# Kernel tuning notes

Hardware: AMD Instinct MI355X
Metric: run time of the kernel (lower is better)

## Reference

```python
import jax, jax.numpy as jnp
import numpy as np


def _splat_one(inp, fx, fy):
    """Bilinear forward-splat one sample.
    inp: [C1, H, W] values to scatter; fx, fy: [H, W] destination coords.
    Returns [C1, H, W] scatter-add accumulation.
    """
    C1, H, W = inp.shape
    inp_flat = inp.reshape(C1, H * W)  # [C1, HW]
    out = jnp.zeros((C1, H * W), dtype=inp.dtype)
    x0 = jnp.floor(fx).astype(jnp.int32)
    y0 = jnp.floor(fy).astype(jnp.int32)
    for dx in (0, 1):
        for dy in (0, 1):
            xi = x0 + dx
            yi = y0 + dy
            # bilinear weight to this corner
            w = (1.0 - jnp.abs(fx - xi.astype(fx.dtype))) * (1.0 - jnp.abs(fy - yi.astype(fy.dtype)))
            valid = (xi >= 0) & (xi < W) & (yi >= 0) & (yi < H)
            w = jnp.where(valid, w, 0.0).reshape(-1)  # [HW]
            idx = (jnp.clip(yi, 0, H - 1) * W + jnp.clip(xi, 0, W - 1)).reshape(-1)
            out = out.at[:, idx].add(inp_flat * w[None, :])
    return out.reshape(C1, H, W)


def softsplat_soft(img, flow, metric):
    """Softmax splatting (FunctionSoftsplat, mode='soft').
    img [B,C,H,W], flow [B,2,H,W] (ch0=x disp, ch1=y disp), metric [B,1,H,W].
    """
    B, C, H, W = img.shape
    weight = jnp.exp(metric)                      # [B,1,H,W]
    inp = jnp.concatenate([img * weight, weight], axis=1)  # [B,C+1,H,W]
    gx = jnp.arange(W, dtype=img.dtype)[None, None, :]
    gy = jnp.arange(H, dtype=img.dtype)[None, :, None]
    fx = flow[:, 0] + gx                          # [B,H,W]
    fy = flow[:, 1] + gy                          # [B,H,W]
    acc = jax.vmap(_splat_one)(inp, fx, fy)       # [B,C+1,H,W]
    norm = acc[:, C:C + 1]
    norm = jnp.where(norm == 0.0, 1.0, norm)      # avoid div-by-zero (matches original)
    return acc[:, :C] / norm


def setup_inputs() -> dict:
    key = jax.random.key(0)
    k1, k2, k3 = jax.random.split(key, 3)
    B, C, H, W = 8, 3, 1024, 1024
    img = jax.random.uniform(k1, (B, C, H, W), dtype=jnp.float32)
    flow = jax.random.normal(k2, (B, 2, H, W), dtype=jnp.float32) * 4.0
    metric = jax.random.normal(k3, (B, 1, H, W), dtype=jnp.float32)
    return {"img": img, "flow": flow, "metric": metric}


def reference(img, flow, metric):
    return softsplat_soft(img, flow, metric)
```

## Files before the change

kernel.cpp:

```cpp
#include <hip/hip_runtime.h>

constexpr int B_ = 8;
constexpr int H_ = 1024;
constexpr int W_ = 1024;
constexpr int HW_ = H_ * W_;

constexpr int TW = 64;
constexpr int TH = 64;
constexpr int R  = 24;
constexpr int WX = TW + 2 * R;
constexpr int WY = TH + 2 * R;
constexpr int NT = 512;
constexpr int LSTRIDE = TW + 1;

__global__ __launch_bounds__(256) void outlier_kernel(
    const float* __restrict__ img,
    const float* __restrict__ flow,
    const float* __restrict__ metric,
    int* __restrict__ counter,
    float4* __restrict__ rec_vals,
    int* __restrict__ rec_cells,
    int cap)
{
    const int t = blockIdx.x * 256 + threadIdx.x;
    if (t >= B_ * HW_) return;
    const int b = t >> 20;
    const int p = t & (HW_ - 1);
    const int y = p >> 10;
    const int x = p & (W_ - 1);

    const float fx = flow[(size_t)(b * 2 + 0) * HW_ + p] + (float)x;
    const float fy = flow[(size_t)(b * 2 + 1) * HW_ + p] + (float)y;
    const float x0f = floorf(fx);
    const float y0f = floorf(fy);
    const int x0 = (int)x0f;
    const int y0 = (int)y0f;

    const bool far = (abs(x0 - x) > R) || (abs(x0 + 1 - x) > R) ||
                     (abs(y0 - y) > R) || (abs(y0 + 1 - y) > R);
    if (!far) return;

    const float wgt = __expf(metric[(size_t)b * HW_ + p]);
    const float v0 = img[(size_t)(b * 3 + 0) * HW_ + p] * wgt;
    const float v1 = img[(size_t)(b * 3 + 1) * HW_ + p] * wgt;
    const float v2 = img[(size_t)(b * 3 + 2) * HW_ + p] * wgt;
    const float wx1 = fx - x0f, wx0 = 1.0f - wx1;
    const float wy1 = fy - y0f, wy0 = 1.0f - wy1;

#pragma unroll
    for (int dy = 0; dy < 2; ++dy) {
        const int yi = y0 + dy;
        if (yi < 0 || yi >= H_) continue;
#pragma unroll
        for (int dx = 0; dx < 2; ++dx) {
            const int xi = x0 + dx;
            if (xi < 0 || xi >= W_) continue;
            if (abs(xi - x) <= R && abs(yi - y) <= R) continue;
            const float w = (dx ? wx1 : wx0) * (dy ? wy1 : wy0);
            const int idx = atomicAdd(counter, 1);
            if (idx < cap) {
                rec_cells[idx] = (b << 20) | (yi << 10) | xi;
                rec_vals[idx]  = make_float4(v0 * w, v1 * w, v2 * w, wgt * w);
            }
        }
    }
}

__global__ __launch_bounds__(NT) void splat_tile_kernel(
    const float* __restrict__ img,
    const float* __restrict__ flow,
    const float* __restrict__ metric,
    float* __restrict__ out,
    const int* __restrict__ counter,
    const float4* __restrict__ rec_vals,
    const int* __restrict__ rec_cells,
    int cap)
{
    __shared__ float acc[4][TH][LSTRIDE];

    const int tid = threadIdx.x;
    const int tx0 = blockIdx.x * TW;
    const int ty0 = blockIdx.y * TH;
    const int b   = blockIdx.z;

    float* const a = &acc[0][0][0];
    for (int i = tid; i < 4 * TH * LSTRIDE; i += NT) a[i] = 0.0f;
    __syncthreads();

    const float* const flowx = flow + (size_t)(b * 2 + 0) * HW_;
    const float* const flowy = flow + (size_t)(b * 2 + 1) * HW_;
    const float* const metr  = metric + (size_t)b * HW_;
    const float* const img0  = img + (size_t)(b * 3 + 0) * HW_;
    const float* const img1  = img + (size_t)(b * 3 + 1) * HW_;
    const float* const img2  = img + (size_t)(b * 3 + 2) * HW_;

    for (int i = tid; i < WX * WY; i += NT) {
        const int wy = i / WX;
        const int wx = i - wy * WX;
        const int sx = tx0 - R + wx;
        const int sy = ty0 - R + wy;
        if (sx < 0 || sx >= W_ || sy < 0 || sy >= H_) continue;
        const int p = (sy << 10) + sx;

        const float fx = flowx[p] + (float)sx;
        const float fy = flowy[p] + (float)sy;
        const float x0f = floorf(fx);
        const float y0f = floorf(fy);
        const int x0 = (int)x0f;
        const int y0 = (int)y0f;

        if (x0 + 1 < tx0 || x0 > tx0 + TW - 1 ||
            y0 + 1 < ty0 || y0 > ty0 + TH - 1) continue;

        const float wgt = __expf(metr[p]);
        const float v0 = img0[p] * wgt;
        const float v1 = img1[p] * wgt;
        const float v2 = img2[p] * wgt;
        const float wx1 = fx - x0f, wx0f_ = 1.0f - wx1;
        const float wy1 = fy - y0f, wy0f_ = 1.0f - wy1;

#pragma unroll
        for (int dy = 0; dy < 2; ++dy) {
            const int yi = y0 + dy;
            const int ly = yi - ty0;
            if ((unsigned)ly >= TH) continue;
#pragma unroll
            for (int dx = 0; dx < 2; ++dx) {
                const int xi = x0 + dx;
                const int lx = xi - tx0;
                if ((unsigned)lx >= TW) continue;
                if (abs(xi - sx) > R || abs(yi - sy) > R) continue;
                const float w = (dx ? wx1 : wx0f_) * (dy ? wy1 : wy0f_);
                atomicAdd(&acc[0][ly][lx], v0 * w);
                atomicAdd(&acc[1][ly][lx], v1 * w);
                atomicAdd(&acc[2][ly][lx], v2 * w);
                atomicAdd(&acc[3][ly][lx], wgt * w);
            }
        }
    }
    __syncthreads();

    const int n = min(*counter, cap);
    for (int r = tid; r < n; r += NT) {
        const int cell = rec_cells[r];
        const int rb = cell >> 20;
        if (rb != b) continue;
        const int q  = cell & (HW_ - 1);
        const int yi = q >> 10;
        const int xi = q & (W_ - 1);
        const int ly = yi - ty0;
        const int lx = xi - tx0;
        if ((unsigned)ly >= TH || (unsigned)lx >= TW) continue;
        const float4 v = rec_vals[r];
        atomicAdd(&acc[0][ly][lx], v.x);
        atomicAdd(&acc[1][ly][lx], v.y);
        atomicAdd(&acc[2][ly][lx], v.z);
        atomicAdd(&acc[3][ly][lx], v.w);
    }
    __syncthreads();

    for (int i = tid; i < TH * TW; i += NT) {
        const int ly = i >> 6;
        const int lx = i & (TW - 1);
        const float wsum = acc[3][ly][lx];
        const float inv = (wsum == 0.0f) ? 1.0f : 1.0f / wsum;
        const int q = ((ty0 + ly) << 10) + (tx0 + lx);
        out[(size_t)(b * 3 + 0) * HW_ + q] = acc[0][ly][lx] * inv;
        out[(size_t)(b * 3 + 1) * HW_ + q] = acc[1][ly][lx] * inv;
        out[(size_t)(b * 3 + 2) * HW_ + q] = acc[2][ly][lx] * inv;
    }
}

extern "C" void kernel_launch(void* const* d_in, const int* in_sizes, int n_in,
                              void* d_out, int out_size, void* d_ws, size_t ws_size,
                              hipStream_t stream)
{
    const float* img    = (const float*)d_in[0];
    const float* flow   = (const float*)d_in[1];
    const float* metric = (const float*)d_in[2];
    float* out = (float*)d_out;

    int* counter = (int*)d_ws;
    long long avail = (long long)ws_size - 64;
    int cap = (int)min((long long)(1 << 22), avail > 0 ? avail / 20 : 0);
    float4* rec_vals = (float4*)((char*)d_ws + 64);
    int* rec_cells = (int*)((char*)d_ws + 64 + (size_t)cap * sizeof(float4));

    hipMemsetAsync(counter, 0, 64, stream);

    {
        const int n = B_ * HW_;
        outlier_kernel<<<(n + 255) / 256, 256, 0, stream>>>(
            img, flow, metric, counter, rec_vals, rec_cells, cap);
    }
    {
        dim3 grid(W_ / TW, H_ / TH, B_);
        splat_tile_kernel<<<grid, NT, 0, stream>>>(
            img, flow, metric, out, counter, rec_vals, rec_cells, cap);
    }
}
```

Before: 710.7 us.

## Precompute fp16-packed weighted values in prepass, shrink halo, vectorize loads and stores

The prepass now also computes exp(metric)-weighted image values and packs them as four fp16 numbers per pixel into a workspace buffer. The tile kernel then reads one 8-byte value and only gathers it for pixels that land in the tile, instead of reading metric plus three image channels. The halo radius drops from 24 to 16, which shrinks the window each tile scans but pushes more pixels into the global outlier list. That list's capacity is also cut to a fixed 65536, which risks silent overflow with flow std 4. Flow loads, prepass loads and output stores are vectorized to float4, and fp16 storage of the weighted values costs precision.

```diff
diff --git a/kernel.cpp b/kernel.cpp
--- a/kernel.cpp
+++ b/kernel.cpp
@@ -1,4 +1,5 @@
 #include <hip/hip_runtime.h>
+#include <hip/hip_fp16.h>
 
 constexpr int B_ = 8;
 constexpr int H_ = 1024;
@@ -7,74 +8,104 @@
 
 constexpr int TW = 64;
 constexpr int TH = 64;
-constexpr int R  = 24;
+constexpr int R  = 16;
 constexpr int WX = TW + 2 * R;
 constexpr int WY = TH + 2 * R;
+constexpr int GPR = WX / 4;
+constexpr int NGROUPS = GPR * WY;
 constexpr int NT = 512;
 constexpr int LSTRIDE = TW + 1;
 
-__global__ __launch_bounds__(256) void outlier_kernel(
+constexpr int CAP = 65536;
+
+constexpr size_t OFF_VALS  = 64;
+constexpr size_t OFF_CELLS = OFF_VALS + (size_t)CAP * 16;
+constexpr size_t OFF_VAL   = OFF_CELLS + (size_t)CAP * 4;
+
+__global__ __launch_bounds__(256) void prepass_kernel(
     const float* __restrict__ img,
     const float* __restrict__ flow,
     const float* __restrict__ metric,
+    uint2* __restrict__ val,
     int* __restrict__ counter,
     float4* __restrict__ rec_vals,
-    int* __restrict__ rec_cells,
-    int cap)
+    int* __restrict__ rec_cells)
 {
     const int t = blockIdx.x * 256 + threadIdx.x;
-    if (t >= B_ * HW_) return;
-    const int b = t >> 20;
-    const int p = t & (HW_ - 1);
-    const int y = p >> 10;
-    const int x = p & (W_ - 1);
-
-    const float fx = flow[(size_t)(b * 2 + 0) * HW_ + p] + (float)x;
-    const float fy = flow[(size_t)(b * 2 + 1) * HW_ + p] + (float)y;
-    const float x0f = floorf(fx);
-    const float y0f = floorf(fy);
-    const int x0 = (int)x0f;
-    const int y0 = (int)y0f;
-
-    const bool far = (abs(x0 - x) > R) || (abs(x0 + 1 - x) > R) ||
-                     (abs(y0 - y) > R) || (abs(y0 + 1 - y) > R);
-    if (!far) return;
-
-    const float wgt = __expf(metric[(size_t)b * HW_ + p]);
-    const float v0 = img[(size_t)(b * 3 + 0) * HW_ + p] * wgt;
-    const float v1 = img[(size_t)(b * 3 + 1) * HW_ + p] * wgt;
-    const float v2 = img[(size_t)(b * 3 + 2) * HW_ + p] * wgt;
-    const float wx1 = fx - x0f, wx0 = 1.0f - wx1;
-    const float wy1 = fy - y0f, wy0 = 1.0f - wy1;
-
-#pragma unroll
-    for (int dy = 0; dy < 2; ++dy) {
-        const int yi = y0 + dy;
-        if (yi < 0 || yi >= H_) continue;
-#pragma unroll
-        for (int dx = 0; dx < 2; ++dx) {
-            const int xi = x0 + dx;
-            if (xi < 0 || xi >= W_) continue;
-            if (abs(xi - x) <= R && abs(yi - y) <= R) continue;
-            const float w = (dx ? wx1 : wx0) * (dy ? wy1 : wy0);
-            const int idx = atomicAdd(counter, 1);
-            if (idx < cap) {
-                rec_cells[idx] = (b << 20) | (yi << 10) | xi;
-                rec_vals[idx]  = make_float4(v0 * w, v1 * w, v2 * w, wgt * w);
+    if (t >= B_ * HW_ / 4) return;
+    const int b  = t >> 18;
+    const int p4 = (t & (HW_ / 4 - 1)) << 2;
+    const int y  = p4 >> 10;
+    const int x0p = p4 & (W_ - 1);
+
+    const float4 m4  = *(const float4*)(metric + (size_t)b * HW_ + p4);
+    const float4 i0  = *(const float4*)(img + (size_t)(b * 3 + 0) * HW_ + p4);
+    const float4 i1  = *(const float4*)(img + (size_t)(b * 3 + 1) * HW_ + p4);
+    const float4 i2  = *(const float4*)(img + (size_t)(b * 3 + 2) * HW_ + p4);
+    const float4 fx4 = *(const float4*)(flow + (size_t)(b * 2 + 0) * HW_ + p4);
+    const float4 fy4 = *(const float4*)(flow + (size_t)(b * 2 + 1) * HW_ + p4);
+
+    uint2 packed[4];
+    const float mv[4] = {m4.x, m4.y, m4.z, m4.w};
+    const float a0[4] = {i0.x, i0.y, i0.z, i0.w};
+    const float a1[4] = {i1.x, i1.y, i1.z, i1.w};
+    const float a2[4] = {i2.x, i2.y, i2.z, i2.w};
+    const float fxa[4] = {fx4.x, fx4.y, fx4.z, fx4.w};
+    const float fya[4] = {fy4.x, fy4.y, fy4.z, fy4.w};
+
+#pragma unroll
+    for (int k = 0; k < 4; ++k) {
+        const float wgt = __expf(mv[k]);
+        const float v0 = a0[k] * wgt;
+        const float v1 = a1[k] * wgt;
+        const float v2 = a2[k] * wgt;
+        const __half2 h01 = __floats2half2_rn(v0, v1);
+        const __half2 h23 = __floats2half2_rn(v2, wgt);
+        packed[k].x = *(const unsigned int*)&h01;
+        packed[k].y = *(const unsigned int*)&h23;
+
+        const int x = x0p + k;
+        const float fx = fxa[k] + (float)x;
+        const float fy = fya[k] + (float)y;
+        const float x0f = floorf(fx);
+        const float y0f = floorf(fy);
+        const int x0 = (int)x0f;
+        const int y0 = (int)y0f;
+        const bool far = (abs(x0 - x) > R) || (abs(x0 + 1 - x) > R) ||
+                         (abs(y0 - y) > R) || (abs(y0 + 1 - y) > R);
+        if (far) {
+            const float wx1 = fx - x0f, wx0 = 1.0f - wx1;
+            const float wy1 = fy - y0f, wy0 = 1.0f - wy1;
+#pragma unroll
+            for (int dy = 0; dy < 2; ++dy) {
+                const int yi = y0 + dy;
+                if (yi < 0 || yi >= H_) continue;
+#pragma unroll
+                for (int dx = 0; dx < 2; ++dx) {
+                    const int xi = x0 + dx;
+                    if (xi < 0 || xi >= W_) continue;
+                    if (abs(xi - x) <= R && abs(yi - y) <= R) continue;
+                    const float w = (dx ? wx1 : wx0) * (dy ? wy1 : wy0);
+                    const int idx = atomicAdd(counter, 1);
+                    if (idx < CAP) {
+                        rec_cells[idx] = (b << 20) | (yi << 10) | xi;
+                        rec_vals[idx]  = make_float4(v0 * w, v1 * w, v2 * w, wgt * w);
+                    }
+                }
             }
         }
     }
+    *(reinterpret_cast<uint4*>(val + (size_t)b * HW_ + p4))     = *(uint4*)&packed[0];
+    *(reinterpret_cast<uint4*>(val + (size_t)b * HW_ + p4) + 1) = *(uint4*)&packed[2];
 }
 
 __global__ __launch_bounds__(NT) void splat_tile_kernel(
-    const float* __restrict__ img,
     const float* __restrict__ flow,
-    const float* __restrict__ metric,
+    const uint2* __restrict__ val,
     float* __restrict__ out,
     const int* __restrict__ counter,
     const float4* __restrict__ rec_vals,
-    const int* __restrict__ rec_cells,
-    int cap)
+    const int* __restrict__ rec_cells)
 {
     __shared__ float acc[4][TH][LSTRIDE];
 
@@ -89,35 +120,23 @@
 
     const float* const flowx = flow + (size_t)(b * 2 + 0) * HW_;
     const float* const flowy = flow + (size_t)(b * 2 + 1) * HW_;
-    const float* const metr  = metric + (size_t)b * HW_;
-    const float* const img0  = img + (size_t)(b * 3 + 0) * HW_;
-    const float* const img1  = img + (size_t)(b * 3 + 1) * HW_;
-    const float* const img2  = img + (size_t)(b * 3 + 2) * HW_;
-
-    for (int i = tid; i < WX * WY; i += NT) {
-        const int wy = i / WX;
-        const int wx = i - wy * WX;
-        const int sx = tx0 - R + wx;
-        const int sy = ty0 - R + wy;
-        if (sx < 0 || sx >= W_ || sy < 0 || sy >= H_) continue;
-        const int p = (sy << 10) + sx;
-
-        const float fx = flowx[p] + (float)sx;
-        const float fy = flowy[p] + (float)sy;
+    const uint2* const valb  = val + (size_t)b * HW_;
+
+    auto process = [&](float fx, float fy, int sx, int sy) {
         const float x0f = floorf(fx);
         const float y0f = floorf(fy);
         const int x0 = (int)x0f;
         const int y0 = (int)y0f;
-
         if (x0 + 1 < tx0 || x0 > tx0 + TW - 1 ||
-            y0 + 1 < ty0 || y0 > ty0 + TH - 1) continue;
-
-        const float wgt = __expf(metr[p]);
-        const float v0 = img0[p] * wgt;
-        const float v1 = img1[p] * wgt;
-        const float v2 = img2[p] * wgt;
-        const float wx1 = fx - x0f, wx0f_ = 1.0f - wx1;
-        const float wy1 = fy - y0f, wy0f_ = 1.0f - wy1;
+            y0 + 1 < ty0 || y0 > ty0 + TH - 1) return;
+
+        const uint2 u = valb[(sy << 10) + sx];
+        const float2 f01 = __half22float2(*(const __half2*)&u.x);
+        const float2 f23 = __half22float2(*(const __half2*)&u.y);
+        const float v0 = f01.x, v1 = f01.y, v2 = f23.x, wgt = f23.y;
+
+        const float wx1 = fx - x0f, wx0 = 1.0f - wx1;
+        const float wy1 = fy - y0f, wy0 = 1.0f - wy1;
 
 #pragma unroll
         for (int dy = 0; dy < 2; ++dy) {
@@ -130,26 +149,38 @@
                 const int lx = xi - tx0;
                 if ((unsigned)lx >= TW) continue;
                 if (abs(xi - sx) > R || abs(yi - sy) > R) continue;
-                const float w = (dx ? wx1 : wx0f_) * (dy ? wy1 : wy0f_);
+                const float w = (dx ? wx1 : wx0) * (dy ? wy1 : wy0);
                 atomicAdd(&acc[0][ly][lx], v0 * w);
                 atomicAdd(&acc[1][ly][lx], v1 * w);
                 atomicAdd(&acc[2][ly][lx], v2 * w);
                 atomicAdd(&acc[3][ly][lx], wgt * w);
             }
         }
+    };
+
+    for (int g = tid; g < NGROUPS; g += NT) {
+        const int row = g / GPR;
+        const int col = g - row * GPR;
+        const int sy = ty0 - R + row;
+        if ((unsigned)sy >= H_) continue;
+        const int gx = tx0 - R + (col << 2);
+        if ((unsigned)gx >= W_) continue;
+        const float4 fx4 = *(const float4*)(flowx + (sy << 10) + gx);
+        const float4 fy4 = *(const float4*)(flowy + (sy << 10) + gx);
+        process(fx4.x + (float)(gx + 0), fy4.x + (float)sy, gx + 0, sy);
+        process(fx4.y + (float)(gx + 1), fy4.y + (float)sy, gx + 1, sy);
+        process(fx4.z + (float)(gx + 2), fy4.z + (float)sy, gx + 2, sy);
+        process(fx4.w + (float)(gx + 3), fy4.w + (float)sy, gx + 3, sy);
     }
     __syncthreads();
 
-    const int n = min(*counter, cap);
+    const int n = min(*counter, CAP);
     for (int r = tid; r < n; r += NT) {
         const int cell = rec_cells[r];
-        const int rb = cell >> 20;
-        if (rb != b) continue;
+        if ((cell >> 20) != b) continue;
         const int q  = cell & (HW_ - 1);
-        const int yi = q >> 10;
-        const int xi = q & (W_ - 1);
-        const int ly = yi - ty0;
-        const int lx = xi - tx0;
+        const int ly = (q >> 10) - ty0;
+        const int lx = (q & (W_ - 1)) - tx0;
         if ((unsigned)ly >= TH || (unsigned)lx >= TW) continue;
         const float4 v = rec_vals[r];
         atomicAdd(&acc[0][ly][lx], v.x);
@@ -159,15 +190,26 @@
     }
     __syncthreads();
 
-    for (int i = tid; i < TH * TW; i += NT) {
-        const int ly = i >> 6;
-        const int lx = i & (TW - 1);
-        const float wsum = acc[3][ly][lx];
-        const float inv = (wsum == 0.0f) ? 1.0f : 1.0f / wsum;
-        const int q = ((ty0 + ly) << 10) + (tx0 + lx);
-        out[(size_t)(b * 3 + 0) * HW_ + q] = acc[0][ly][lx] * inv;
-        out[(size_t)(b * 3 + 1) * HW_ + q] = acc[1][ly][lx] * inv;
-        out[(size_t)(b * 3 + 2) * HW_ + q] = acc[2][ly][lx] * inv;
+    for (int i = tid; i < TH * TW / 4; i += NT) {
+        const int ly  = i >> 4;
+        const int lx  = (i & 15) << 2;
+        float4 o0, o1, o2;
+        float invs[4];
+#pragma unroll
+        for (int k = 0; k < 4; ++k) {
+            const float wsum = acc[3][ly][lx + k];
+            invs[k] = (wsum == 0.0f) ? 1.0f : 1.0f / wsum;
+        }
+        o0 = make_float4(acc[0][ly][lx] * invs[0], acc[0][ly][lx+1] * invs[1],
+                         acc[0][ly][lx+2] * invs[2], acc[0][ly][lx+3] * invs[3]);
+        o1 = make_float4(acc[1][ly][lx] * invs[0], acc[1][ly][lx+1] * invs[1],
+                         acc[1][ly][lx+2] * invs[2], acc[1][ly][lx+3] * invs[3]);
+        o2 = make_float4(acc[2][ly][lx] * invs[0], acc[2][ly][lx+1] * invs[1],
+                         acc[2][ly][lx+2] * invs[2], acc[2][ly][lx+3] * invs[3]);
+        const int q = ((ty0 + ly) << 10) + tx0 + lx;
+        *(float4*)(out + (size_t)(b * 3 + 0) * HW_ + q) = o0;
+        *(float4*)(out + (size_t)(b * 3 + 1) * HW_ + q) = o1;
+        *(float4*)(out + (size_t)(b * 3 + 2) * HW_ + q) = o2;
     }
 }
 
@@ -180,22 +222,21 @@
     const float* metric = (const float*)d_in[2];
     float* out = (float*)d_out;
 
-    int* counter = (int*)d_ws;
-    long long avail = (long long)ws_size - 64;
-    int cap = (int)min((long long)(1 << 22), avail > 0 ? avail / 20 : 0);
-    float4* rec_vals = (float4*)((char*)d_ws + 64);
-    int* rec_cells = (int*)((char*)d_ws + 64 + (size_t)cap * sizeof(float4));
+    int*    counter   = (int*)d_ws;
+    float4* rec_vals  = (float4*)((char*)d_ws + OFF_VALS);
+    int*    rec_cells = (int*)((char*)d_ws + OFF_CELLS);
+    uint2*  val       = (uint2*)((char*)d_ws + OFF_VAL);
 
     hipMemsetAsync(counter, 0, 64, stream);
 
     {
-        const int n = B_ * HW_;
-        outlier_kernel<<<(n + 255) / 256, 256, 0, stream>>>(
-            img, flow, metric, counter, rec_vals, rec_cells, cap);
+        const int n = B_ * HW_ / 4;
+        prepass_kernel<<<(n + 255) / 256, 256, 0, stream>>>(
+            img, flow, metric, val, counter, rec_vals, rec_cells);
     }
     {
         dim3 grid(W_ / TW, H_ / TH, B_);
         splat_tile_kernel<<<grid, NT, 0, stream>>>(
-            img, flow, metric, out, counter, rec_vals, rec_cells, cap);
+            flow, val, out, counter, rec_vals, rec_cells);
     }
 }
```

Measured after the change: 738.2 us. 3.9% more time.
